# Optimization experiments

Hardware: AMD Instinct MI355X
Metric: run time of the kernel (lower is better)

## Reference

```python
import jax, jax.numpy as jnp
import numpy as np

EMB = 1024
HID = 4096
B = 2
T = 4096
NUM_BLOCK = 24
EPS = 1e-6


def rmsnorm(x):
    # unparameterized RMS normalization over last dim
    return x * jax.lax.rsqrt(jnp.mean(jnp.square(x), axis=-1, keepdims=True) + EPS)


def setup_inputs() -> dict:
    key = jax.random.key(0)
    k1, k2, k3, k4 = jax.random.split(key, 4)
    x = jax.random.normal(k1, (B, T, EMB), dtype=jnp.float32)
    W1 = 0.02 * jax.random.normal(k2, (HID, EMB), dtype=jnp.float32)
    W2 = 0.02 * jax.random.normal(k3, (HID, EMB), dtype=jnp.float32)
    W3 = (0.02 / np.sqrt(NUM_BLOCK)) * jax.random.normal(k4, (EMB, HID), dtype=jnp.float32)
    return {"x": x, "W1": W1, "W2": W2, "W3": W3}


def bar_quadratic_causal_preact_stable(a, b):
    # y_t = (1/t^2) * sum_{i<=t} sum_{j<=t} exp(a_i + b_j), per feature channel.
    # exp factorizes, so compute stably via log-cumsum-exp along the seq axis.
    seq = a.shape[1]
    log_t = jnp.log(jnp.arange(1, seq + 1, dtype=a.dtype))  # [T]
    la = jax.lax.cumlogsumexp(a, axis=1)  # [B,T,H]
    lb = jax.lax.cumlogsumexp(b, axis=1)  # [B,T,H]
    return jnp.exp(la + lb - 2.0 * log_t[None, :, None])


def reference(x, W1, W2, W3):
    r = rmsnorm(x)
    a = jnp.einsum('bte,he->bth', r, W1)  # fc_1, no bias
    b = jnp.einsum('bte,he->bth', r, W2)  # fc_2, no bias
    r = bar_quadratic_causal_preact_stable(a, b)
    r = rmsnorm(r)
    r = jnp.einsum('bth,eh->bte', r, W3)  # fc_3, no bias
    return x + r
```

## Files before the change

kernel.cpp:

```cpp
#include <hip/hip_runtime.h>

#define EMB 1024
#define HID 4096
#define NB 2
#define TT 4096
#define MROWS (NB*TT)
#define N1 (2*HID)
#define CHUNK 128
#define NCH 32

typedef short short8 __attribute__((ext_vector_type(8)));
typedef float v4f   __attribute__((ext_vector_type(4)));

__device__ __forceinline__ unsigned short f2bf(float f) {
  unsigned int u = __float_as_uint(f);
  u += 0x7FFFu + ((u >> 16) & 1u);
  return (unsigned short)(u >> 16);
}
__device__ __forceinline__ float bf2f(unsigned short s) {
  return __uint_as_float(((unsigned int)s) << 16);
}
__device__ __forceinline__ void g2l16(const void* g, void* l) {
  __builtin_amdgcn_global_load_lds(
      (const __attribute__((address_space(1))) void*)g,
      (__attribute__((address_space(3))) void*)l, 16, 0, 0);
}

__device__ __forceinline__ float block_reduce_sum(float v, float* sbuf) {
  #pragma unroll
  for (int off = 32; off; off >>= 1) v += __shfl_down(v, off, 64);
  int lane = threadIdx.x & 63, w = threadIdx.x >> 6;
  if (lane == 0) sbuf[w] = v;
  __syncthreads();
  return sbuf[0] + sbuf[1] + sbuf[2] + sbuf[3];
}

__global__ __launch_bounds__(256) void conv_w12(const float* __restrict__ W1,
                                                const float* __restrict__ W2,
                                                unsigned short* __restrict__ o) {
  size_t i = ((size_t)blockIdx.x*256 + threadIdx.x)*4;
  const float* s = (i < (size_t)HID*EMB) ? (W1 + i) : (W2 + (i - (size_t)HID*EMB));
  float4 v = *(const float4*)s;
  ushort4 u; u.x=f2bf(v.x); u.y=f2bf(v.y); u.z=f2bf(v.z); u.w=f2bf(v.w);
  *(ushort4*)(o + i) = u;
}
__global__ __launch_bounds__(256) void conv_w3(const float* __restrict__ W3,
                                               unsigned short* __restrict__ o) {
  size_t i = ((size_t)blockIdx.x*256 + threadIdx.x)*4;
  float4 v = *(const float4*)(W3 + i);
  ushort4 u; u.x=f2bf(v.x); u.y=f2bf(v.y); u.z=f2bf(v.z); u.w=f2bf(v.w);
  *(ushort4*)(o + i) = u;
}

__global__ __launch_bounds__(256) void rmsnorm_x(const float* __restrict__ x,
                                                 unsigned short* __restrict__ r) {
  __shared__ float sbuf[4];
  int row = blockIdx.x;
  float4 v = *(const float4*)(x + (size_t)row*EMB + threadIdx.x*4);
  float ss = v.x*v.x + v.y*v.y + v.z*v.z + v.w*v.w;
  float tot = block_reduce_sum(ss, sbuf);
  float sc = rsqrtf(tot * (1.0f/EMB) + 1e-6f);
  ushort4 o; o.x=f2bf(v.x*sc); o.y=f2bf(v.y*sc); o.z=f2bf(v.z*sc); o.w=f2bf(v.w*sc);
  *(ushort4*)(r + (size_t)row*EMB + threadIdx.x*4) = o;
}

__global__ __launch_bounds__(256) void rowssq(const unsigned short* __restrict__ y,
                                              float* __restrict__ sc) {
  __shared__ float sbuf[4];
  int row = blockIdx.x;
  const unsigned short* p = y + (size_t)row*HID + threadIdx.x*16;
  short8 v0 = *(const short8*)p;
  short8 v1 = *(const short8*)(p+8);
  float ss = 0.f;
  #pragma unroll
  for (int j=0;j<8;++j){ float a=bf2f((unsigned short)v0[j]), b=bf2f((unsigned short)v1[j]); ss += a*a + b*b; }
  float tot = block_reduce_sum(ss, sbuf);
  if (threadIdx.x == 0) sc[row] = rsqrtf(tot*(1.0f/HID) + 1e-6f);
}

template<int MODE>
__global__ __launch_bounds__(256, 2)
void gemm_bt(const unsigned short* __restrict__ A,
             const unsigned short* __restrict__ Bt,
             unsigned short* __restrict__ Ch,
             float* __restrict__ Cf,
             const float* __restrict__ X,
             const float* __restrict__ Sc,
             float* __restrict__ part,
             int K, int N) {
  __shared__ short lA[128*64];
  __shared__ short lB[128*64];
  __shared__ float cs[2][128];
  const int tid  = threadIdx.x;
  const int lane = tid & 63;
  const int wm   = (tid >> 6) >> 1, wn = (tid >> 6) & 1;
  const int rowBase = blockIdx.y * 128;
  const int colBase = blockIdx.x * 128;

  v4f acc[4][4];
  #pragma unroll
  for (int i=0;i<4;++i)
    #pragma unroll
    for (int j=0;j<4;++j) acc[i][j] = (v4f){0.f,0.f,0.f,0.f};

  for (int k0 = 0; k0 < K; k0 += 64) {
    #pragma unroll
    for (int j = 0; j < 4; ++j) {
      int s = j*256 + tid;
      int m = s >> 3;
      int c = (s & 7) ^ (m & 7);
      g2l16(A + (size_t)(rowBase + m)*K + k0 + c*8, &lA[s*8]);
    }
    #pragma unroll
    for (int j = 0; j < 4; ++j) {
      int s = j*256 + tid;
      int m = s >> 3;
      int c = (s & 7) ^ (m & 7);
      g2l16(Bt + (size_t)(colBase + m)*K + k0 + c*8, &lB[s*8]);
    }
    __syncthreads();
    #pragma unroll
    for (int s2 = 0; s2 < 2; ++s2) {
      const int quad = lane >> 4;
      const int cc = s2*4 + quad;
      short8 aF[4], bF[4];
      #pragma unroll
      for (int mt = 0; mt < 4; ++mt) {
        int ml = wm*64 + mt*16 + (lane & 15);
        aF[mt] = *(const short8*)&lA[(ml*8 + (cc ^ (ml & 7)))*8];
      }
      #pragma unroll
      for (int nt = 0; nt < 4; ++nt) {
        int nl = wn*64 + nt*16 + (lane & 15);
        bF[nt] = *(const short8*)&lB[(nl*8 + (cc ^ (nl & 7)))*8];
      }
      #pragma unroll
      for (int mt = 0; mt < 4; ++mt)
        #pragma unroll
        for (int nt = 0; nt < 4; ++nt)
          acc[mt][nt] = __builtin_amdgcn_mfma_f32_16x16x32_bf16(aF[mt], bF[nt], acc[mt][nt], 0, 0, 0);
    }
    __syncthreads();
  }

  const int quad = lane >> 4, c15 = lane & 15;
  float csum[4] = {0.f, 0.f, 0.f, 0.f};
  #pragma unroll
  for (int mt = 0; mt < 4; ++mt) {
    #pragma unroll
    for (int nt = 0; nt < 4; ++nt) {
      int col = colBase + wn*64 + nt*16 + c15;
      #pragma unroll
      for (int r = 0; r < 4; ++r) {
        int row = rowBase + wm*64 + mt*16 + quad*4 + r;
        size_t idx = (size_t)row*N + col;
        float v = acc[mt][nt][r];
        if (MODE == 0) {
          float e = __expf(v);
          _Float16 h = (_Float16)e;
          Ch[idx] = *(unsigned short*)&h;
          csum[nt] += e;
        } else {
          Cf[idx] = Sc[row]*v + X[idx];
        }
      }
    }
  }
  if (MODE == 0) {
    #pragma unroll
    for (int nt = 0; nt < 4; ++nt) {
      float s = csum[nt];
      s += __shfl_xor(s, 16, 64);
      s += __shfl_xor(s, 32, 64);
      if (lane < 16) cs[wm][wn*64 + nt*16 + lane] = s;
    }
    __syncthreads();
    if (tid < 128)
      part[(size_t)(colBase + tid)*64 + blockIdx.y] = cs[0][tid] + cs[1][tid];
  }
}

__global__ __launch_bounds__(256) void scan_prefix(float* __restrict__ part) {
  int idx = blockIdx.x*256 + threadIdx.x;
  int col = idx >> 1, bb = idx & 1;
  float* p = part + (size_t)col*64 + bb*NCH;
  float run = 0.f;
  #pragma unroll
  for (int c = 0; c < NCH; ++c) { float v = p[c]; p[c] = run; run += v; }
}

__global__ __launch_bounds__(256) void scan_emit(const unsigned short* __restrict__ ab,
                                                 const float* __restrict__ part,
                                                 unsigned short* __restrict__ y) {
  int h = blockIdx.x*256 + threadIdx.x;
  int cy = blockIdx.y, bb = blockIdx.z;
  float sa = part[(size_t)h*64 + bb*NCH + cy];
  float sb = part[(size_t)(HID + h)*64 + bb*NCH + cy];
  const unsigned short* pa = ab + ((size_t)(bb*TT + cy*CHUNK))*N1 + h;
  const unsigned short* pb = pa + HID;
  unsigned short* py = y + ((size_t)(bb*TT + cy*CHUNK))*HID + h;
  int t0 = cy*CHUNK;
  #pragma unroll 4
  for (int i = 0; i < CHUNK; ++i) {
    unsigned short ua = pa[(size_t)i*N1];
    unsigned short ub = pb[(size_t)i*N1];
    sa += (float)(*(const _Float16*)&ua);
    sb += (float)(*(const _Float16*)&ub);
    float inv = 1.0f / (float)(t0 + i + 1);
    py[(size_t)i*HID] = f2bf(sa*sb*inv*inv);
  }
}

extern "C" void kernel_launch(void* const* d_in, const int* in_sizes, int n_in,
                              void* d_out, int out_size, void* d_ws, size_t ws_size,
                              hipStream_t stream) {
  const float* x  = (const float*)d_in[0];
  const float* W1 = (const float*)d_in[1];
  const float* W2 = (const float*)d_in[2];
  const float* W3 = (const float*)d_in[3];
  float* out = (float*)d_out;
  char* ws = (char*)d_ws;

  unsigned short* r_bf   = (unsigned short*)(ws);
  unsigned short* w12_bf = (unsigned short*)(ws + 16777216ull);
  unsigned short* w3_bf  = (unsigned short*)(ws + 33554432ull);
  unsigned short* ab_h   = (unsigned short*)(ws + 41943040ull);
  unsigned short* y_bf   = (unsigned short*)(ws + 176160768ull);
  float*          sc     = (float*)(ws + 41943040ull);
  float*          part   = (float*)d_out;

  conv_w12<<<8192, 256, 0, stream>>>(W1, W2, w12_bf);
  conv_w3<<<4096, 256, 0, stream>>>(W3, w3_bf);
  rmsnorm_x<<<MROWS, 256, 0, stream>>>(x, r_bf);
  gemm_bt<0><<<dim3(64,64), 256, 0, stream>>>(r_bf, w12_bf, ab_h, nullptr, nullptr, nullptr, part, EMB, N1);
  scan_prefix<<<64, 256, 0, stream>>>(part);
  scan_emit<<<dim3(16,NCH,2), 256, 0, stream>>>(ab_h, part, y_bf);
  rowssq<<<MROWS, 256, 0, stream>>>(y_bf, sc);
  gemm_bt<1><<<dim3(8,64), 256, 0, stream>>>(y_bf, w3_bf, nullptr, out, x, sc, nullptr, HID, EMB);
}
```

Measured before the change: 411.0 us.

## Split-K the output GEMM with atomics, merge weight conversions, drop scan_prefix

The final GEMM is split four ways along K (grid z=4, 1024 each) and accumulates into the output with float atomic adds, after a new init_out kernel copies x into out. The point is to fill the GPU better, since the old grid had only 512 blocks. The two weight-conversion kernels are merged into one launch, and the prefix-scan kernel is removed: each scan_emit block now sums its own chunk prefix serially. The costs are atomic traffic, an extra pass over x to initialise the output, and redundant prefix work per block. The sc buffer moves to a separate workspace offset.

```diff
diff --git a/kernel.cpp b/kernel.cpp
--- a/kernel.cpp
+++ b/kernel.cpp
@@ -35,21 +35,19 @@
   return sbuf[0] + sbuf[1] + sbuf[2] + sbuf[3];
 }
 
-__global__ __launch_bounds__(256) void conv_w12(const float* __restrict__ W1,
+__global__ __launch_bounds__(256) void conv_all(const float* __restrict__ W1,
                                                 const float* __restrict__ W2,
-                                                unsigned short* __restrict__ o) {
+                                                const float* __restrict__ W3,
+                                                unsigned short* __restrict__ o12,
+                                                unsigned short* __restrict__ o3) {
   size_t i = ((size_t)blockIdx.x*256 + threadIdx.x)*4;
-  const float* s = (i < (size_t)HID*EMB) ? (W1 + i) : (W2 + (i - (size_t)HID*EMB));
+  const float* s; unsigned short* d;
+  if (i < (size_t)HID*EMB)        { s = W1 + i;                      d = o12 + i; }
+  else if (i < 2ull*HID*EMB)      { s = W2 + (i - (size_t)HID*EMB);  d = o12 + i; }
+  else                            { s = W3 + (i - 2ull*HID*EMB);     d = o3 + (i - 2ull*HID*EMB); }
   float4 v = *(const float4*)s;
   ushort4 u; u.x=f2bf(v.x); u.y=f2bf(v.y); u.z=f2bf(v.z); u.w=f2bf(v.w);
-  *(ushort4*)(o + i) = u;
-}
-__global__ __launch_bounds__(256) void conv_w3(const float* __restrict__ W3,
-                                               unsigned short* __restrict__ o) {
-  size_t i = ((size_t)blockIdx.x*256 + threadIdx.x)*4;
-  float4 v = *(const float4*)(W3 + i);
-  ushort4 u; u.x=f2bf(v.x); u.y=f2bf(v.y); u.z=f2bf(v.z); u.w=f2bf(v.w);
-  *(ushort4*)(o + i) = u;
+  *(ushort4*)d = u;
 }
 
 __global__ __launch_bounds__(256) void rmsnorm_x(const float* __restrict__ x,
@@ -78,16 +76,21 @@
   if (threadIdx.x == 0) sc[row] = rsqrtf(tot*(1.0f/HID) + 1e-6f);
 }
 
+__global__ __launch_bounds__(256) void init_out(const float* __restrict__ x,
+                                                float* __restrict__ o) {
+  size_t i = ((size_t)blockIdx.x*256 + threadIdx.x)*4;
+  *(float4*)(o + i) = *(const float4*)(x + i);
+}
+
 template<int MODE>
 __global__ __launch_bounds__(256, 2)
 void gemm_bt(const unsigned short* __restrict__ A,
              const unsigned short* __restrict__ Bt,
              unsigned short* __restrict__ Ch,
              float* __restrict__ Cf,
-             const float* __restrict__ X,
              const float* __restrict__ Sc,
              float* __restrict__ part,
-             int K, int N) {
+             int K, int KCH, int N) {
   __shared__ short lA[128*64];
   __shared__ short lB[128*64];
   __shared__ float cs[2][128];
@@ -96,6 +99,7 @@
   const int wm   = (tid >> 6) >> 1, wn = (tid >> 6) & 1;
   const int rowBase = blockIdx.y * 128;
   const int colBase = blockIdx.x * 128;
+  const int kStart  = blockIdx.z * KCH;
 
   v4f acc[4][4];
   #pragma unroll
@@ -103,7 +107,7 @@
     #pragma unroll
     for (int j=0;j<4;++j) acc[i][j] = (v4f){0.f,0.f,0.f,0.f};
 
-  for (int k0 = 0; k0 < K; k0 += 64) {
+  for (int k0 = kStart; k0 < kStart + KCH; k0 += 64) {
     #pragma unroll
     for (int j = 0; j < 4; ++j) {
       int s = j*256 + tid;
@@ -161,7 +165,7 @@
           Ch[idx] = *(unsigned short*)&h;
           csum[nt] += e;
         } else {
-          Cf[idx] = Sc[row]*v + X[idx];
+          unsafeAtomicAdd(&Cf[idx], Sc[row]*v);
         }
       }
     }
@@ -180,22 +184,15 @@
   }
 }
 
-__global__ __launch_bounds__(256) void scan_prefix(float* __restrict__ part) {
-  int idx = blockIdx.x*256 + threadIdx.x;
-  int col = idx >> 1, bb = idx & 1;
-  float* p = part + (size_t)col*64 + bb*NCH;
-  float run = 0.f;
-  #pragma unroll
-  for (int c = 0; c < NCH; ++c) { float v = p[c]; p[c] = run; run += v; }
-}
-
 __global__ __launch_bounds__(256) void scan_emit(const unsigned short* __restrict__ ab,
                                                  const float* __restrict__ part,
                                                  unsigned short* __restrict__ y) {
   int h = blockIdx.x*256 + threadIdx.x;
   int cy = blockIdx.y, bb = blockIdx.z;
-  float sa = part[(size_t)h*64 + bb*NCH + cy];
-  float sb = part[(size_t)(HID + h)*64 + bb*NCH + cy];
+  const float* pp = part + (size_t)h*64 + bb*NCH;
+  const float* pq = part + (size_t)(HID + h)*64 + bb*NCH;
+  float sa = 0.f, sb = 0.f;
+  for (int c = 0; c < cy; ++c) { sa += pp[c]; sb += pq[c]; }
   const unsigned short* pa = ab + ((size_t)(bb*TT + cy*CHUNK))*N1 + h;
   const unsigned short* pb = pa + HID;
   unsigned short* py = y + ((size_t)(bb*TT + cy*CHUNK))*HID + h;
@@ -226,15 +223,14 @@
   unsigned short* w3_bf  = (unsigned short*)(ws + 33554432ull);
   unsigned short* ab_h   = (unsigned short*)(ws + 41943040ull);
   unsigned short* y_bf   = (unsigned short*)(ws + 176160768ull);
-  float*          sc     = (float*)(ws + 41943040ull);
+  float*          sc     = (float*)(ws + 243269632ull);
   float*          part   = (float*)d_out;
 
-  conv_w12<<<8192, 256, 0, stream>>>(W1, W2, w12_bf);
-  conv_w3<<<4096, 256, 0, stream>>>(W3, w3_bf);
+  conv_all<<<12288, 256, 0, stream>>>(W1, W2, W3, w12_bf, w3_bf);
   rmsnorm_x<<<MROWS, 256, 0, stream>>>(x, r_bf);
-  gemm_bt<0><<<dim3(64,64), 256, 0, stream>>>(r_bf, w12_bf, ab_h, nullptr, nullptr, nullptr, part, EMB, N1);
-  scan_prefix<<<64, 256, 0, stream>>>(part);
+  gemm_bt<0><<<dim3(64,64,1), 256, 0, stream>>>(r_bf, w12_bf, ab_h, nullptr, nullptr, part, EMB, EMB, N1);
   scan_emit<<<dim3(16,NCH,2), 256, 0, stream>>>(ab_h, part, y_bf);
   rowssq<<<MROWS, 256, 0, stream>>>(y_bf, sc);
-  gemm_bt<1><<<dim3(8,64), 256, 0, stream>>>(y_bf, w3_bf, nullptr, out, x, sc, nullptr, HID, EMB);
-}
+  init_out<<<8192, 256, 0, stream>>>(x, out);
+  gemm_bt<1><<<dim3(8,64,4), 256, 0, stream>>>(y_bf, w3_bf, nullptr, out, sc, nullptr, HID, 1024, EMB);
+}
```

Result: slower. 489.6 us (+19.1%).
